# Kernel tuning notes

Measured on AMD Instinct MI355X. Metric: run time of the kernel, lower is better.

The kernel has to match this reference:

```python
import jax, jax.numpy as jnp
import numpy as np

DG = 4      # deformable groups
PAD = 1     # (kernel_size - 1) // 2
KH = KW = 3


def deform_conv(x, offset, weight, dg=DG, pad=PAD):
    """DCN v1 (mmcv layout): offset channels = dg * 2 * K, per group ordered
    (y0, x0, y1, x1, ...) over kernel points in row-major order.
    x: [B, C, H, W]; offset: [B, dg*2*K, H, W]; weight: [Cout, C, kh, kw].
    """
    B, C, H, W = x.shape
    Cout, Cin, kh, kw = weight.shape
    K = kh * kw
    Cg = C // dg
    off = offset.reshape(B, dg, K, 2, H, W)

    ys = jnp.arange(H, dtype=x.dtype)
    xs = jnp.arange(W, dtype=x.dtype)
    kyy = jnp.repeat(jnp.arange(kh, dtype=x.dtype) - pad, kw)   # [K]
    kxx = jnp.tile(jnp.arange(kw, dtype=x.dtype) - pad, kh)     # [K]

    # fractional sampling positions, [B, dg, K, H, W]
    py = ys[None, :, None] + kyy[:, None, None] + off[:, :, :, 0]
    px = xs[None, None, :] + kxx[:, None, None] + off[:, :, :, 1]

    y0 = jnp.floor(py)
    x0 = jnp.floor(px)
    ty = py - y0
    tx = px - x0
    y1 = y0 + 1.0
    x1 = x0 + 1.0

    x_flat = x.reshape(B, dg, Cg, H * W)
    acc = jnp.zeros((B, dg, Cg, K, H, W), dtype=x.dtype)
    corners = [
        (y0, x0, (1.0 - ty) * (1.0 - tx)),
        (y0, x1, (1.0 - ty) * tx),
        (y1, x0, ty * (1.0 - tx)),
        (y1, x1, ty * tx),
    ]
    for yc, xc, wgt in corners:
        valid = (yc >= 0) & (yc <= H - 1) & (xc >= 0) & (xc <= W - 1)
        yi = jnp.clip(yc, 0, H - 1).astype(jnp.int32)
        xi = jnp.clip(xc, 0, W - 1).astype(jnp.int32)
        idx = (yi * W + xi).reshape(B, dg, 1, K * H * W)
        v = jnp.take_along_axis(x_flat, idx, axis=3).reshape(B, dg, Cg, K, H, W)
        wv = jnp.where(valid, wgt, 0.0)[:, :, None]  # [B, dg, 1, K, H, W]
        acc = acc + v * wv

    w = weight.reshape(Cout, dg, Cg, kh * kw)
    return jnp.einsum('bgckhw,ogck->bohw', acc, w)


def setup_inputs() -> dict:
    key = jax.random.key(0)
    ks = jax.random.split(key, 6)
    B, C, H, W = 8, 256, 64, 64
    return {
        'reg_feat': jax.random.normal(ks[0], (B, C, H, W), jnp.float32),
        'cls_feat': jax.random.normal(ks[1], (B, C, H, W), jnp.float32),
        'pred_init': jax.random.normal(ks[2], (B, 34, H, W), jnp.float32),
        'w_offset': jax.random.normal(ks[3], (DG * 2 * KH * KW, 34), jnp.float32) * 0.1,
        'w_reg': jax.random.normal(ks[4], (C, C, KH, KW), jnp.float32) * 0.01,
        'w_cls': jax.random.normal(ks[5], (C, C, KH, KW), jnp.float32) * 0.01,
    }


def reference(reg_feat, cls_feat, pred_init, w_offset, w_reg, w_cls):
    # 1x1 offset conv on detached anchor-shape prediction
    offset = jnp.einsum('bchw,oc->bohw', jax.lax.stop_gradient(pred_init), w_offset)
    reg_refine = jax.nn.relu(deform_conv(reg_feat, offset, w_reg))
    cls_refine = jax.nn.relu(deform_conv(cls_feat, offset, w_cls))
    return (reg_refine, cls_refine)
```

## Files before the change

kernel.cpp:

```cpp
#include <hip/hip_runtime.h>

#define B_   8
#define C_   256
#define HW_  4096
#define OC_  72
#define PC_  34
#define CLS_OFF (B_ * C_ * HW_)

typedef __attribute__((ext_vector_type(8))) short short8v;
typedef __attribute__((ext_vector_type(4))) float f32x4;

__device__ __forceinline__ ushort f2bf(float f) {
  uint u = __float_as_uint(f);
  return (ushort)((u + 0x7fffu + ((u >> 16) & 1u)) >> 16);
}
__device__ __forceinline__ float bf2f(ushort h) {
  return __uint_as_float(((uint)h) << 16);
}

__global__ __launch_bounds__(256)
void prep_kernel(const float* __restrict__ pred, const float* __restrict__ wo,
                 const float* __restrict__ w_reg, const float* __restrict__ w_cls,
                 float* __restrict__ offset, ushort* __restrict__ wpk) {
  if (blockIdx.x < 128) {
    const int p  = blockIdx.x * 256 + threadIdx.x;
    const int b  = p >> 12;
    const int hw = p & 4095;
    const float* pp = pred + (size_t)b * PC_ * HW_ + hw;
    float v[PC_];
#pragma unroll
    for (int i = 0; i < PC_; ++i) v[i] = pp[(size_t)i * HW_];
    float* op = offset + (size_t)b * OC_ * HW_ + hw;
    for (int o = 0; o < OC_; ++o) {
      float s = 0.f;
#pragma unroll
      for (int i = 0; i < PC_; ++i) s = fmaf(v[i], wo[o * PC_ + i], s);
      op[(size_t)o * HW_] = s;
    }
  } else {
    const int tid = (blockIdx.x - 128) * 256 + threadIdx.x;
    const int l   = tid & 63;
    const int mf  = (tid >> 6) & 15;
    int rest = tid >> 10;
    const int kk  = rest & 1; rest >>= 1;
    const int s   = rest % 36;
    const int map = rest / 36;
    const float* src = map ? w_cls : w_reg;
    const int g = s / 9, kp = s % 9;
    const int o = mf * 16 + (l & 15);
    const int cbase = kk * 32 + (l >> 4) * 8;
    union { ushort u[8]; short8v v; } hu, lu;
#pragma unroll
    for (int j = 0; j < 8; ++j) {
      const int c = cbase + j;
      const float v = src[o * 2304 + (g * 64 + c) * 9 + kp];
      const ushort h = f2bf(v);
      hu.u[j] = h;
      lu.u[j] = f2bf(v - bf2f(h));
    }
    const size_t eb = ((size_t)((map * 36 + s) * 2 + kk)) * 16384 + mf * 512 + l * 8;
    *reinterpret_cast<short8v*>(wpk + eb)        = hu.v;
    *reinterpret_cast<short8v*>(wpk + eb + 8192) = lu.v;
  }
}

__device__ __forceinline__ void calcp(float oy, float ox, int ss, int yy, int xx,
                                      int& i0, int& i1, int& i2, int& i3,
                                      float& w0, float& w1, float& w2, float& w3) {
  const int kp = ss % 9;
  const float py  = (float)(yy + kp / 3 - 1) + oy;
  const float pxx = (float)(xx + kp % 3 - 1) + ox;
  const float y0f = floorf(py), x0f = floorf(pxx);
  const float ty = py - y0f, tx = pxx - x0f;
  const int y0 = (int)y0f, x0 = (int)x0f;
  const int y1 = y0 + 1, x1 = x0 + 1;
  const bool vy0 = (y0 >= 0) & (y0 <= 63), vy1 = (y1 >= 0) & (y1 <= 63);
  const bool vx0 = (x0 >= 0) & (x0 <= 63), vx1 = (x1 >= 0) & (x1 <= 63);
  const int cy0 = min(max(y0, 0), 63), cy1 = min(max(y1, 0), 63);
  const int cx0 = min(max(x0, 0), 63), cx1 = min(max(x1, 0), 63);
  i0 = cy0 * 64 + cx0;  w0 = (vy0 && vx0) ? (1.f - ty) * (1.f - tx) : 0.f;
  i1 = cy0 * 64 + cx1;  w1 = (vy0 && vx1) ? (1.f - ty) * tx         : 0.f;
  i2 = cy1 * 64 + cx0;  w2 = (vy1 && vx0) ? ty * (1.f - tx)         : 0.f;
  i3 = cy1 * 64 + cx1;  w3 = (vy1 && vx1) ? ty * tx                 : 0.f;
}

__global__ __launch_bounds__(256, 2)
void deform_mfma(const float* __restrict__ xreg, const float* __restrict__ xcls,
                 const float* __restrict__ off, const ushort* __restrict__ wpk,
                 float* __restrict__ out) {
  __shared__ ushort Bh[2][4096];
  __shared__ ushort Bl[2][4096];

  const int lin = blockIdx.y * 512 + blockIdx.x;
  const int nid = (lin & 7) * 128 + (lin >> 3);
  const int map = nid >> 9;
  const int nt  = nid & 511;
  const int b   = nt >> 6;
  const int yy  = nt & 63;
  const int px0 = yy * 64;

  const int t = threadIdx.x;
  const int lane = t & 63, wid = t >> 6;
  const int px = t & 63;
  const int kgb = wid;
  const float* xsrc = map ? xcls : xreg;

  f32x4 acc[4][4];
#pragma unroll
  for (int mf = 0; mf < 4; ++mf)
#pragma unroll
    for (int nf = 0; nf < 4; ++nf) acc[mf][nf] = (f32x4){0.f, 0.f, 0.f, 0.f};

  const size_t obidx = ((size_t)b * OC_) * HW_ + px0 + px;
  float offY = off[obidx];
  float offX = off[obidx + HW_];

  {
    int i0, i1, i2, i3; float w0, w1, w2, w3;
    calcp(offY, offX, 0, yy, px, i0, i1, i2, i3, w0, w1, w2, w3);
    const float* xb = xsrc + ((size_t)(b * 4 * 64 + kgb * 8)) * HW_;
    float rc0[16], rc1[16], rc2[16], rc3[16];
#pragma unroll
    for (int q = 0; q < 2; ++q)
#pragma unroll
      for (int i = 0; i < 8; ++i) {
        const float* xc = xb + (size_t)(q * 32 + i) * HW_;
        rc0[q * 8 + i] = xc[i0]; rc1[q * 8 + i] = xc[i1];
        rc2[q * 8 + i] = xc[i2]; rc3[q * 8 + i] = xc[i3];
      }
    offY = off[obidx + 2 * HW_];
    offX = off[obidx + 3 * HW_];
#pragma unroll
    for (int q = 0; q < 2; ++q) {
      union { ushort u[8]; short8v v; } hu, lu;
#pragma unroll
      for (int i = 0; i < 8; ++i) {
        const float v = w0 * rc0[q * 8 + i] + w1 * rc1[q * 8 + i]
                      + w2 * rc2[q * 8 + i] + w3 * rc3[q * 8 + i];
        const ushort h = f2bf(v);
        hu.u[i] = h; lu.u[i] = f2bf(v - bf2f(h));
      }
      const int slot = (q * 4 + (px >> 4)) * 64 + kgb * 16 + (px & 15);
      *reinterpret_cast<short8v*>(&Bh[0][slot * 8]) = hu.v;
      *reinterpret_cast<short8v*>(&Bl[0][slot * 8]) = lu.v;
    }
  }
  __syncthreads();

  for (int s = 0; s < 36; ++s) {
    const int cb = s & 1, nb = cb ^ 1;

    short8v a_h[2][4], a_l[2][4];
    const size_t abase = ((size_t)(map * 36 + s)) * 32768 + (size_t)lane * 8;
#pragma unroll
    for (int kk = 0; kk < 2; ++kk)
#pragma unroll
      for (int mf = 0; mf < 4; ++mf) {
        const size_t e = abase + (size_t)kk * 16384 + (size_t)(wid * 4 + mf) * 512;
        a_h[kk][mf] = *reinterpret_cast<const short8v*>(wpk + e);
        a_l[kk][mf] = *reinterpret_cast<const short8v*>(wpk + e + 8192);
      }

    int i0, i1, i2, i3; float w0, w1, w2, w3;
    float rc0[16], rc1[16], rc2[16], rc3[16];
    if (s < 35) {
      calcp(offY, offX, s + 1, yy, px, i0, i1, i2, i3, w0, w1, w2, w3);
      const int g1 = (s + 1) / 9;
      const float* xb = xsrc + ((size_t)((b * 4 + g1) * 64 + kgb * 8)) * HW_;
#pragma unroll
      for (int q = 0; q < 2; ++q)
#pragma unroll
        for (int i = 0; i < 8; ++i) {
          const float* xc = xb + (size_t)(q * 32 + i) * HW_;
          rc0[q * 8 + i] = xc[i0]; rc1[q * 8 + i] = xc[i1];
          rc2[q * 8 + i] = xc[i2]; rc3[q * 8 + i] = xc[i3];
        }
      if (s < 34) {
        offY = off[obidx + (size_t)(2 * s + 4) * HW_];
        offX = off[obidx + (size_t)(2 * s + 5) * HW_];
      }
    }

    __builtin_amdgcn_s_setprio(1);
#pragma unroll
    for (int kk = 0; kk < 2; ++kk)
#pragma unroll
      for (int nf = 0; nf < 4; ++nf) {
        const short8v bh = *reinterpret_cast<const short8v*>(&Bh[cb][((kk * 4 + nf) * 64 + lane) * 8]);
        const short8v bl = *reinterpret_cast<const short8v*>(&Bl[cb][((kk * 4 + nf) * 64 + lane) * 8]);
#pragma unroll
        for (int mf = 0; mf < 4; ++mf) {
          f32x4 c = acc[mf][nf];
          c = __builtin_amdgcn_mfma_f32_16x16x32_bf16(a_l[kk][mf], bh, c, 0, 0, 0);
          c = __builtin_amdgcn_mfma_f32_16x16x32_bf16(a_h[kk][mf], bl, c, 0, 0, 0);
          c = __builtin_amdgcn_mfma_f32_16x16x32_bf16(a_h[kk][mf], bh, c, 0, 0, 0);
          acc[mf][nf] = c;
        }
      }
    __builtin_amdgcn_s_setprio(0);

    if (s < 35) {
#pragma unroll
      for (int q = 0; q < 2; ++q) {
        union { ushort u[8]; short8v v; } hu, lu;
#pragma unroll
        for (int i = 0; i < 8; ++i) {
          const float v = w0 * rc0[q * 8 + i] + w1 * rc1[q * 8 + i]
                        + w2 * rc2[q * 8 + i] + w3 * rc3[q * 8 + i];
          const ushort h = f2bf(v);
          hu.u[i] = h; lu.u[i] = f2bf(v - bf2f(h));
        }
        const int slot = (q * 4 + (px >> 4)) * 64 + kgb * 16 + (px & 15);
        *reinterpret_cast<short8v*>(&Bh[nb][slot * 8]) = hu.v;
        *reinterpret_cast<short8v*>(&Bl[nb][slot * 8]) = lu.v;
      }
    }
    __syncthreads();
  }

  float* obase = out + (map ? CLS_OFF : 0) + (size_t)b * C_ * HW_ + px0;
  const int m0 = wid * 64;
#pragma unroll
  for (int mf = 0; mf < 4; ++mf)
#pragma unroll
    for (int nf = 0; nf < 4; ++nf)
#pragma unroll
      for (int r = 0; r < 4; ++r) {
        const int o = m0 + mf * 16 + (lane >> 4) * 4 + r;
        const int n = nf * 16 + (lane & 15);
        obase[(size_t)o * HW_ + n] = fmaxf(acc[mf][nf][r], 0.f);
      }
}

extern "C" void kernel_launch(void* const* d_in, const int* in_sizes, int n_in,
                              void* d_out, int out_size, void* d_ws, size_t ws_size,
                              hipStream_t stream) {
  const float* reg_feat = (const float*)d_in[0];
  const float* cls_feat = (const float*)d_in[1];
  const float* pred     = (const float*)d_in[2];
  const float* w_off    = (const float*)d_in[3];
  const float* w_reg    = (const float*)d_in[4];
  const float* w_cls    = (const float*)d_in[5];
  float* outp = (float*)d_out;

  float*  offset = (float*)d_ws;
  ushort* wpk    = (ushort*)((char*)d_ws + (size_t)B_ * OC_ * HW_ * 4);

  prep_kernel<<<dim3(704), 256, 0, stream>>>(pred, w_off, w_reg, w_cls,
                                             offset, wpk);
  deform_mfma<<<dim3(512, 2), dim3(256), 0, stream>>>(reg_feat, cls_feat,
                                                      offset, wpk, outp);
}
```

Before: 623.1 us.

## Drop LDS double buffering and register prefetch to raise occupancy to three blocks

Replaces the software-pipelined loop, which prefetched the next step's bilinear gather into 64 registers and double-buffered the LDS B tile, with a single-buffered loop. Each step now gathers, interpolates and writes LDS, syncs, then runs the MFMAs. A-fragment loads are split per kk to shrink live registers, and bf16 packing uses the paired hardware conversion. Launch bounds ask for three blocks per CU so that more resident waves hide gather latency. The trade-off is losing intra-block overlap of gather and MFMA and adding a second barrier per step.

```diff
diff --git a/kernel.cpp b/kernel.cpp
--- a/kernel.cpp
+++ b/kernel.cpp
@@ -1,4 +1,5 @@
 #include <hip/hip_runtime.h>
+#include <hip/hip_bf16.h>
 
 #define B_   8
 #define C_   256
@@ -16,6 +17,11 @@
 }
 __device__ __forceinline__ float bf2f(ushort h) {
   return __uint_as_float(((uint)h) << 16);
+}
+__device__ __forceinline__ uint pk2(float v0, float v1) {
+  union { __hip_bfloat162 b; uint u; } c;
+  c.b = __float22bfloat162_rn(float2{v0, v1});
+  return c.u;
 }
 
 __global__ __launch_bounds__(256)
@@ -84,12 +90,12 @@
   i3 = cy1 * 64 + cx1;  w3 = (vy1 && vx1) ? ty * tx                 : 0.f;
 }
 
-__global__ __launch_bounds__(256, 2)
+__global__ __launch_bounds__(256, 3)
 void deform_mfma(const float* __restrict__ xreg, const float* __restrict__ xcls,
                  const float* __restrict__ off, const ushort* __restrict__ wpk,
                  float* __restrict__ out) {
-  __shared__ ushort Bh[2][4096];
-  __shared__ ushort Bl[2][4096];
+  __shared__ ushort Bh[4096];
+  __shared__ ushort Bl[4096];
 
   const int lin = blockIdx.y * 512 + blockIdx.x;
   const int nid = (lin & 7) * 128 + (lin >> 3);
@@ -115,107 +121,77 @@
   float offY = off[obidx];
   float offX = off[obidx + HW_];
 
-  {
+  for (int s = 0; s < 36; ++s) {
     int i0, i1, i2, i3; float w0, w1, w2, w3;
-    calcp(offY, offX, 0, yy, px, i0, i1, i2, i3, w0, w1, w2, w3);
-    const float* xb = xsrc + ((size_t)(b * 4 * 64 + kgb * 8)) * HW_;
-    float rc0[16], rc1[16], rc2[16], rc3[16];
-#pragma unroll
-    for (int q = 0; q < 2; ++q)
-#pragma unroll
-      for (int i = 0; i < 8; ++i) {
-        const float* xc = xb + (size_t)(q * 32 + i) * HW_;
-        rc0[q * 8 + i] = xc[i0]; rc1[q * 8 + i] = xc[i1];
-        rc2[q * 8 + i] = xc[i2]; rc3[q * 8 + i] = xc[i3];
-      }
-    offY = off[obidx + 2 * HW_];
-    offX = off[obidx + 3 * HW_];
+    calcp(offY, offX, s, yy, px, i0, i1, i2, i3, w0, w1, w2, w3);
+
+    const int g = s / 9;
+    const float* xb = xsrc + ((size_t)((b * 4 + g) * 64 + kgb * 8)) * HW_;
+
+    __syncthreads();
+
 #pragma unroll
     for (int q = 0; q < 2; ++q) {
-      union { ushort u[8]; short8v v; } hu, lu;
-#pragma unroll
-      for (int i = 0; i < 8; ++i) {
-        const float v = w0 * rc0[q * 8 + i] + w1 * rc1[q * 8 + i]
-                      + w2 * rc2[q * 8 + i] + w3 * rc3[q * 8 + i];
-        const ushort h = f2bf(v);
-        hu.u[i] = h; lu.u[i] = f2bf(v - bf2f(h));
-      }
+      const float* xq = xb + (size_t)q * 32 * HW_;
       const int slot = (q * 4 + (px >> 4)) * 64 + kgb * 16 + (px & 15);
-      *reinterpret_cast<short8v*>(&Bh[0][slot * 8]) = hu.v;
-      *reinterpret_cast<short8v*>(&Bl[0][slot * 8]) = lu.v;
-    }
-  }
-  __syncthreads();
-
-  for (int s = 0; s < 36; ++s) {
-    const int cb = s & 1, nb = cb ^ 1;
-
-    short8v a_h[2][4], a_l[2][4];
-    const size_t abase = ((size_t)(map * 36 + s)) * 32768 + (size_t)lane * 8;
-#pragma unroll
-    for (int kk = 0; kk < 2; ++kk)
+#pragma unroll
+      for (int h = 0; h < 2; ++h) {
+        float r0[4], r1[4], r2[4], r3[4];
+#pragma unroll
+        for (int i = 0; i < 4; ++i) {
+          const float* xc = xq + (size_t)(h * 4 + i) * HW_;
+          r0[i] = xc[i0]; r1[i] = xc[i1]; r2[i] = xc[i2]; r3[i] = xc[i3];
+        }
+        uint hh[2], ll[2];
+#pragma unroll
+        for (int p = 0; p < 2; ++p) {
+          const float v0 = fmaf(w0, r0[2 * p],     fmaf(w1, r1[2 * p],     fmaf(w2, r2[2 * p],     w3 * r3[2 * p])));
+          const float v1 = fmaf(w0, r0[2 * p + 1], fmaf(w1, r1[2 * p + 1], fmaf(w2, r2[2 * p + 1], w3 * r3[2 * p + 1])));
+          const uint hu = pk2(v0, v1);
+          const float l0 = v0 - __uint_as_float(hu << 16);
+          const float l1 = v1 - __uint_as_float(hu & 0xffff0000u);
+          hh[p] = hu;
+          ll[p] = pk2(l0, l1);
+        }
+        *reinterpret_cast<uint2*>(&Bh[slot * 8 + h * 4]) = make_uint2(hh[0], hh[1]);
+        *reinterpret_cast<uint2*>(&Bl[slot * 8 + h * 4]) = make_uint2(ll[0], ll[1]);
+      }
+    }
+
+    if (s < 35) {
+      offY = off[obidx + (size_t)(2 * s + 2) * HW_];
+      offX = off[obidx + (size_t)(2 * s + 3) * HW_];
+    }
+
+    __syncthreads();
+
+    __builtin_amdgcn_s_setprio(1);
+#pragma unroll
+    for (int kk = 0; kk < 2; ++kk) {
+      short8v a_h[4], a_l[4];
+      const size_t abase = ((size_t)(map * 36 + s)) * 32768
+                         + (size_t)kk * 16384 + (size_t)lane * 8;
 #pragma unroll
       for (int mf = 0; mf < 4; ++mf) {
-        const size_t e = abase + (size_t)kk * 16384 + (size_t)(wid * 4 + mf) * 512;
-        a_h[kk][mf] = *reinterpret_cast<const short8v*>(wpk + e);
-        a_l[kk][mf] = *reinterpret_cast<const short8v*>(wpk + e + 8192);
-      }
-
-    int i0, i1, i2, i3; float w0, w1, w2, w3;
-    float rc0[16], rc1[16], rc2[16], rc3[16];
-    if (s < 35) {
-      calcp(offY, offX, s + 1, yy, px, i0, i1, i2, i3, w0, w1, w2, w3);
-      const int g1 = (s + 1) / 9;
-      const float* xb = xsrc + ((size_t)((b * 4 + g1) * 64 + kgb * 8)) * HW_;
-#pragma unroll
-      for (int q = 0; q < 2; ++q)
-#pragma unroll
-        for (int i = 0; i < 8; ++i) {
-          const float* xc = xb + (size_t)(q * 32 + i) * HW_;
-          rc0[q * 8 + i] = xc[i0]; rc1[q * 8 + i] = xc[i1];
-          rc2[q * 8 + i] = xc[i2]; rc3[q * 8 + i] = xc[i3];
-        }
-      if (s < 34) {
-        offY = off[obidx + (size_t)(2 * s + 4) * HW_];
-        offX = off[obidx + (size_t)(2 * s + 5) * HW_];
-      }
-    }
-
-    __builtin_amdgcn_s_setprio(1);
-#pragma unroll
-    for (int kk = 0; kk < 2; ++kk)
+        const size_t e = abase + (size_t)(wid * 4 + mf) * 512;
+        a_h[mf] = *reinterpret_cast<const short8v*>(wpk + e);
+        a_l[mf] = *reinterpret_cast<const short8v*>(wpk + e + 8192);
+      }
 #pragma unroll
       for (int nf = 0; nf < 4; ++nf) {
-        const short8v bh = *reinterpret_cast<const short8v*>(&Bh[cb][((kk * 4 + nf) * 64 + lane) * 8]);
-        const short8v bl = *reinterpret_cast<const short8v*>(&Bl[cb][((kk * 4 + nf) * 64 + lane) * 8]);
+        const short8v bh = *reinterpret_cast<const short8v*>(&Bh[((kk * 4 + nf) * 64 + lane) * 8]);
+        const short8v bl = *reinterpret_cast<const short8v*>(&Bl[((kk * 4 + nf) * 64 + lane) * 8]);
 #pragma unroll
         for (int mf = 0; mf < 4; ++mf) {
           f32x4 c = acc[mf][nf];
-          c = __builtin_amdgcn_mfma_f32_16x16x32_bf16(a_l[kk][mf], bh, c, 0, 0, 0);
-          c = __builtin_amdgcn_mfma_f32_16x16x32_bf16(a_h[kk][mf], bl, c, 0, 0, 0);
-          c = __builtin_amdgcn_mfma_f32_16x16x32_bf16(a_h[kk][mf], bh, c, 0, 0, 0);
+          c = __builtin_amdgcn_mfma_f32_16x16x32_bf16(a_l[mf], bh, c, 0, 0, 0);
+          c = __builtin_amdgcn_mfma_f32_16x16x32_bf16(a_h[mf], bl, c, 0, 0, 0);
+          c = __builtin_amdgcn_mfma_f32_16x16x32_bf16(a_h[mf], bh, c, 0, 0, 0);
           acc[mf][nf] = c;
         }
       }
+    }
     __builtin_amdgcn_s_setprio(0);
-
-    if (s < 35) {
-#pragma unroll
-      for (int q = 0; q < 2; ++q) {
-        union { ushort u[8]; short8v v; } hu, lu;
-#pragma unroll
-        for (int i = 0; i < 8; ++i) {
-          const float v = w0 * rc0[q * 8 + i] + w1 * rc1[q * 8 + i]
-                        + w2 * rc2[q * 8 + i] + w3 * rc3[q * 8 + i];
-          const ushort h = f2bf(v);
-          hu.u[i] = h; lu.u[i] = f2bf(v - bf2f(h));
-        }
-        const int slot = (q * 4 + (px >> 4)) * 64 + kgb * 16 + (px & 15);
-        *reinterpret_cast<short8v*>(&Bh[nb][slot * 8]) = hu.v;
-        *reinterpret_cast<short8v*>(&Bl[nb][slot * 8]) = lu.v;
-      }
-    }
-    __syncthreads();
   }
 
   float* obase = out + (map ? CLS_OFF : 0) + (size_t)b * C_ * HW_ + px0;
```

New measurement: 598.1 us. 1.04x faster.
